# Kernel optimization log

Measured on AMD Instinct MI355X. Metric: run time of the kernel, lower is better.

## Reference

```python
import jax, jax.numpy as jnp
import numpy as np

B, T, E = 2, 2048, 1024
H = 16
DH = E // H  # 64
DFF = 4 * E
EPS = 1e-5


def _layernorm(x, gamma, beta):
    mu = jnp.mean(x, axis=-1, keepdims=True)
    var = jnp.mean((x - mu) ** 2, axis=-1, keepdims=True)
    return (x - mu) * jax.lax.rsqrt(var + EPS) * gamma + beta


def setup_inputs() -> dict:
    key = jax.random.key(0)
    ks = jax.random.split(key, 16)
    s_e = 1.0 / np.sqrt(E)
    s_f = 1.0 / np.sqrt(DFF)
    return {
        "x": jax.random.normal(ks[0], (B, T, E), jnp.float32),
        # per-head QKV projections, stacked over heads [H, E, DH]
        "Wq": jax.random.normal(ks[1], (H, E, DH), jnp.float32) * s_e,
        "bq": jnp.zeros((H, DH), jnp.float32),
        "Wk": jax.random.normal(ks[2], (H, E, DH), jnp.float32) * s_e,
        "bk": jnp.zeros((H, DH), jnp.float32),
        "Wv": jax.random.normal(ks[3], (H, E, DH), jnp.float32) * s_e,
        "bv": jnp.zeros((H, DH), jnp.float32),
        # output projection
        "Wo": jax.random.normal(ks[4], (E, E), jnp.float32) * s_e,
        "bo": jnp.zeros((E,), jnp.float32),
        # feed-forward
        "W1": jax.random.normal(ks[5], (E, DFF), jnp.float32) * s_e,
        "b1": jnp.zeros((DFF,), jnp.float32),
        "W2": jax.random.normal(ks[6], (DFF, E), jnp.float32) * s_f,
        "b2": jnp.zeros((E,), jnp.float32),
        # layernorms
        "gamma1": jnp.ones((E,), jnp.float32),
        "beta1": jnp.zeros((E,), jnp.float32),
        "gamma2": jnp.ones((E,), jnp.float32),
        "beta2": jnp.zeros((E,), jnp.float32),
    }


def reference(x, Wq, bq, Wk, bk, Wv, bv, Wo, bo, W1, b1, W2, b2,
              gamma1, beta1, gamma2, beta2):
    Bc, Tc, Ec = x.shape
    # --- multi-head causal self-attention (dropout = eval/identity) ---
    xn = _layernorm(x, gamma1, beta1)
    q = jnp.einsum('bte,hed->bhtd', xn, Wq) + bq[:, None, :]
    k = jnp.einsum('bte,hed->bhtd', xn, Wk) + bk[:, None, :]
    v = jnp.einsum('bte,hed->bhtd', xn, Wv) + bv[:, None, :]
    scale = 1.0 / np.sqrt(q.shape[-1])
    scores = jnp.einsum('bhtd,bhsd->bhts', q, k) * scale  # [B,H,T,T]
    causal = jnp.tril(jnp.ones((Tc, Tc), bool))
    scores = jnp.where(causal, scores, jnp.float32(-1e9))
    attn = jax.nn.softmax(scores, axis=-1)
    out = jnp.einsum('bhts,bhsd->bhtd', attn, v)          # [B,H,T,DH]
    out = out.transpose(0, 2, 1, 3).reshape(Bc, Tc, Ec)    # concat heads
    out = out @ Wo + bo
    x = x + out
    # --- feed-forward ---
    xn2 = _layernorm(x, gamma2, beta2)
    h = jax.nn.relu(xn2 @ W1 + b1)
    x = x + (h @ W2 + b2)
    return x
```

## Files before the change

kernel.cpp:

```cpp
#include <hip/hip_runtime.h>
#include <stdint.h>

#define BT    4096
#define EDIM  1024
#define TLEN  2048
#define NH    16
#define DHH   64
#define DFFN  4096

typedef short short8 __attribute__((ext_vector_type(8)));
typedef float f32x4  __attribute__((ext_vector_type(4)));

__device__ __forceinline__ float bf2f(unsigned short u) {
    union { unsigned int i; float f; } c; c.i = ((unsigned int)u) << 16; return c.f;
}
__device__ __forceinline__ unsigned short f2bf(float f) {
    union { float f; unsigned int i; } c; c.f = f;
    unsigned int u = c.i;
    unsigned int r = u + 0x7fffu + ((u >> 16) & 1u);
    return (unsigned short)(r >> 16);
}

template<int QKV>
__global__ __launch_bounds__(256) void transpose_kernel(
    const float* src, unsigned short* dst, int Kdim, int srcStride)
{
    __shared__ float T[64][65];
    int t = threadIdx.x;
    int n0 = blockIdx.x * 64, k0 = blockIdx.y * 64;
    int r = t >> 4, c4 = (t & 15) * 4;
    #pragma unroll
    for (int i = 0; i < 4; i++) {
        int rr = r + i * 16;
        const float* p;
        if (QKV) p = src + ((size_t)(n0 >> 6)) * 65536 + (size_t)(k0 + rr) * 64 + c4;
        else     p = src + (size_t)(k0 + rr) * srcStride + n0 + c4;
        float4 v = *(const float4*)p;
        T[c4 + 0][rr] = v.x;
        T[c4 + 1][rr] = v.y;
        T[c4 + 2][rr] = v.z;
        T[c4 + 3][rr] = v.w;
    }
    __syncthreads();
    int rn = t >> 2, ck = (t & 3) * 16;
    short8 o0, o1;
    #pragma unroll
    for (int j = 0; j < 8; j++) o0[j] = (short)f2bf(T[rn][ck + j]);
    #pragma unroll
    for (int j = 0; j < 8; j++) o1[j] = (short)f2bf(T[rn][ck + 8 + j]);
    unsigned short* dp = dst + (size_t)(n0 + rn) * Kdim + k0 + ck;
    *(short8*)dp       = o0;
    *(short8*)(dp + 8) = o1;
}

template<int F32IN>
__global__ __launch_bounds__(256) void ln_stats_kernel(
    const void* __restrict__ x, float* __restrict__ mu_out, float* __restrict__ rstd_out)
{
    int row = blockIdx.x, tid = threadIdx.x;
    size_t off = (size_t)row * EDIM + tid * 4;
    float v0, v1, v2, v3;
    if (F32IN) {
        float4 a = *(const float4*)((const float*)x + off);
        v0 = a.x; v1 = a.y; v2 = a.z; v3 = a.w;
    } else {
        ushort4 raw = *(const ushort4*)((const unsigned short*)x + off);
        v0 = bf2f(raw.x); v1 = bf2f(raw.y); v2 = bf2f(raw.z); v3 = bf2f(raw.w);
    }
    float s  = v0 + v1 + v2 + v3;
    float ss = v0*v0 + v1*v1 + v2*v2 + v3*v3;
    #pragma unroll
    for (int o = 1; o < 64; o <<= 1) {
        s  += __shfl_xor(s,  o, 64);
        ss += __shfl_xor(ss, o, 64);
    }
    __shared__ float red[8];
    int wave = tid >> 6;
    if ((tid & 63) == 0) { red[wave*2] = s; red[wave*2+1] = ss; }
    __syncthreads();
    if (tid == 0) {
        s  = red[0] + red[2] + red[4] + red[6];
        ss = red[1] + red[3] + red[5] + red[7];
        float mu  = s * (1.0f / EDIM);
        float var = ss * (1.0f / EDIM) - mu * mu;
        mu_out[row]   = mu;
        rstd_out[row] = rsqrtf(var + 1e-5f);
    }
}

template<int F32IN>
__global__ __launch_bounds__(256) void ln_apply_kernel(
    const void* __restrict__ x, const float* __restrict__ mu, const float* __restrict__ rstd,
    const float* __restrict__ g, const float* __restrict__ b, unsigned short* __restrict__ out)
{
    int row = blockIdx.x, tid = threadIdx.x;
    float m = mu[row], rs = rstd[row];
    size_t off = (size_t)row * EDIM + tid * 4;
    float v0, v1, v2, v3;
    if (F32IN) {
        float4 a = *(const float4*)((const float*)x + off);
        v0 = a.x; v1 = a.y; v2 = a.z; v3 = a.w;
    } else {
        ushort4 raw = *(const ushort4*)((const unsigned short*)x + off);
        v0 = bf2f(raw.x); v1 = bf2f(raw.y); v2 = bf2f(raw.z); v3 = bf2f(raw.w);
    }
    float4 gv = *(const float4*)(g + tid * 4);
    float4 bv = *(const float4*)(b + tid * 4);
    ushort4 o;
    o.x = f2bf((v0 - m) * rs * gv.x + bv.x);
    o.y = f2bf((v1 - m) * rs * gv.y + bv.y);
    o.z = f2bf((v2 - m) * rs * gv.z + bv.z);
    o.w = f2bf((v3 - m) * rs * gv.w + bv.w);
    *(ushort4*)(out + off) = o;
}

#define V_QKV  0
#define V_WO   1
#define V_FF1  2
#define V_FF2A 3
#define V_FF2B 4
#define LDKK 72

template<int VARIANT, int BN>
__global__ __launch_bounds__(256) void gemm_bt_kernel(
    const unsigned short* A,
    const unsigned short* Bt,
    const float* bias,
    const void* resid,
    void* out,
    int N, int K)
{
    constexpr int NJ = BN / 32;
    __shared__ __align__(16) unsigned short As[128 * LDKK];
    __shared__ __align__(16) unsigned short Bs[BN * LDKK];
    int tid  = threadIdx.x;
    int lane = tid & 63, wave = tid >> 6;
    int quad = lane >> 4, l16 = lane & 15;
    int wr = wave >> 1, wc = wave & 1;
    int m0 = blockIdx.y * 128, n0 = blockIdx.x * BN;

    f32x4 acc[4][NJ];
    #pragma unroll
    for (int i = 0; i < 4; i++)
        #pragma unroll
        for (int j = 0; j < NJ; j++) acc[i][j] = (f32x4){0.f, 0.f, 0.f, 0.f};

    int rowA = tid >> 1, colA = (tid & 1) * 32;
    int rowB, colB;
    if (BN == 128) { rowB = tid >> 1; colB = (tid & 1) * 32; }
    else           { rowB = tid >> 2; colB = (tid & 3) * 16; }

    for (int k0 = 0; k0 < K; k0 += 64) {
        const unsigned short* ap = A + (size_t)(m0 + rowA) * K + k0 + colA;
        short8 a0 = *(const short8*)ap;
        short8 a1 = *(const short8*)(ap + 8);
        short8 a2 = *(const short8*)(ap + 16);
        short8 a3 = *(const short8*)(ap + 24);
        const unsigned short* bp = Bt + (size_t)(n0 + rowB) * K + k0 + colB;
        short8 b0 = *(const short8*)bp;
        short8 b1 = *(const short8*)(bp + 8);
        short8 b2, b3;
        if (BN == 128) {
            b2 = *(const short8*)(bp + 16);
            b3 = *(const short8*)(bp + 24);
        }

        *(short8*)(&As[rowA * LDKK + colA])      = a0;
        *(short8*)(&As[rowA * LDKK + colA + 8])  = a1;
        *(short8*)(&As[rowA * LDKK + colA + 16]) = a2;
        *(short8*)(&As[rowA * LDKK + colA + 24]) = a3;
        *(short8*)(&Bs[rowB * LDKK + colB])      = b0;
        *(short8*)(&Bs[rowB * LDKK + colB + 8])  = b1;
        if (BN == 128) {
            *(short8*)(&Bs[rowB * LDKK + colB + 16]) = b2;
            *(short8*)(&Bs[rowB * LDKK + colB + 24]) = b3;
        }

        __syncthreads();

        #pragma unroll
        for (int ks = 0; ks < 2; ks++) {
            short8 af[4], bf[NJ];
            #pragma unroll
            for (int i = 0; i < 4; i++)
                af[i] = *(const short8*)(&As[(wr * 64 + i * 16 + l16) * LDKK + ks * 32 + quad * 8]);
            #pragma unroll
            for (int j = 0; j < NJ; j++)
                bf[j] = *(const short8*)(&Bs[(wc * (BN / 2) + j * 16 + l16) * LDKK + ks * 32 + quad * 8]);
            #pragma unroll
            for (int i = 0; i < 4; i++)
                #pragma unroll
                for (int j = 0; j < NJ; j++)
                    acc[i][j] = __builtin_amdgcn_mfma_f32_16x16x32_bf16(af[i], bf[j], acc[i][j], 0, 0, 0);
        }

        __syncthreads();
    }

    #pragma unroll
    for (int j = 0; j < NJ; j++) {
        int c = n0 + wc * (BN / 2) + j * 16 + l16;
        float bi = (VARIANT == V_FF2A) ? 0.0f : bias[c];
        #pragma unroll
        for (int i = 0; i < 4; i++) {
            #pragma unroll
            for (int r = 0; r < 4; r++) {
                int m = m0 + wr * 64 + i * 16 + quad * 4 + r;
                float val = acc[i][j][r] + bi;
                if (VARIANT == V_WO)
                    val += ((const float*)resid)[(size_t)m * N + c];
                if (VARIANT == V_FF2B)
                    val += bf2f(((const unsigned short*)resid)[(size_t)m * N + c])
                         + ((const float*)out)[(size_t)m * N + c];
                if (VARIANT == V_FF1)
                    val = fmaxf(val, 0.0f);
                if (VARIANT == V_QKV) {
                    int b = m >> 11, t = m & 2047, h = c >> 6, d = c & 63;
                    ((unsigned short*)out)[(((size_t)(b * NH + h)) * TLEN + t) * DHH + d] = f2bf(val);
                } else if (VARIANT == V_FF2A || VARIANT == V_FF2B) {
                    ((float*)out)[(size_t)m * N + c] = val;
                } else {
                    ((unsigned short*)out)[(size_t)m * N + c] = f2bf(val);
                }
            }
        }
    }
}

__global__ __launch_bounds__(256) void attn_kernel(
    const unsigned short* __restrict__ q,
    const unsigned short* __restrict__ k,
    const unsigned short* __restrict__ v,
    unsigned short* __restrict__ att)
{
    __shared__ __align__(16) unsigned short Ks[64 * 72];
    __shared__ __align__(16) unsigned short Vt[64 * 72];
    __shared__ __align__(16) unsigned short Ps[4][16 * 72];
    int tid  = threadIdx.x;
    int lane = tid & 63, wave = tid >> 6;
    int quad = lane >> 4, l16 = lane & 15;
    int bh = blockIdx.x;
    int q0 = blockIdx.y * 64;
    int qw = q0 + wave * 16;

    const unsigned short* Qb = q + ((size_t)bh * TLEN + qw) * DHH;
    const unsigned short* Kb = k + (size_t)bh * TLEN * DHH;
    const unsigned short* Vb = v + (size_t)bh * TLEN * DHH;

    short8 aq0 = *(const short8*)(Qb + l16 * DHH + quad * 8);
    short8 aq1 = *(const short8*)(Qb + l16 * DHH + 32 + quad * 8);

    f32x4 o[4];
    #pragma unroll
    for (int n = 0; n < 4; n++) o[n] = (f32x4){0.f, 0.f, 0.f, 0.f};
    f32x4 mrow = {-1e30f, -1e30f, -1e30f, -1e30f};
    f32x4 lrow = {0.f, 0.f, 0.f, 0.f};
    unsigned short* Pw = Ps[wave];

    int krow = tid >> 2, kcol = (tid & 3) * 16;
    int vsl  = tid >> 5, vd2  = (tid & 31) * 2;

    int nch = blockIdx.y + 1;
    for (int ch = 0; ch < nch; ch++) {
        int s0 = ch * 64;
        __syncthreads();
        {
            const unsigned short* kp = Kb + (size_t)(s0 + krow) * DHH + kcol;
            *(short8*)(&Ks[krow * 72 + kcol])     = *(const short8*)kp;
            *(short8*)(&Ks[krow * 72 + kcol + 8]) = *(const short8*)(kp + 8);
        }
        #pragma unroll
        for (int i = 0; i < 8; i++) {
            int sl = vsl + i * 8;
            ushort2 w = *(const ushort2*)(Vb + (size_t)(s0 + sl) * DHH + vd2);
            Vt[vd2 * 72 + sl]       = w.x;
            Vt[(vd2 + 1) * 72 + sl] = w.y;
        }
        __syncthreads();

        f32x4 S[4];
        #pragma unroll
        for (int n = 0; n < 4; n++) {
            S[n] = (f32x4){0.f, 0.f, 0.f, 0.f};
            short8 b0 = *(const short8*)(&Ks[(n * 16 + l16) * 72 + quad * 8]);
            short8 b1 = *(const short8*)(&Ks[(n * 16 + l16) * 72 + 32 + quad * 8]);
            S[n] = __builtin_amdgcn_mfma_f32_16x16x32_bf16(aq0, b0, S[n], 0, 0, 0);
            S[n] = __builtin_amdgcn_mfma_f32_16x16x32_bf16(aq1, b1, S[n], 0, 0, 0);
        }

        int qbase = qw + quad * 4;
        #pragma unroll
        for (int r = 0; r < 4; r++) {
            float xv[4];
            #pragma unroll
            for (int n = 0; n < 4; n++) {
                float xx = S[n][r] * 0.125f;
                if (s0 + n * 16 + l16 > qbase + r) xx = -1e30f;
                xv[n] = xx;
            }
            float mx = fmaxf(fmaxf(xv[0], xv[1]), fmaxf(xv[2], xv[3]));
            mx = fmaxf(mx, __shfl_xor(mx, 1, 64));
            mx = fmaxf(mx, __shfl_xor(mx, 2, 64));
            mx = fmaxf(mx, __shfl_xor(mx, 4, 64));
            mx = fmaxf(mx, __shfl_xor(mx, 8, 64));
            float mnew  = fmaxf(mrow[r], mx);
            float alpha = __expf(mrow[r] - mnew);
            float p0 = __expf(xv[0] - mnew);
            float p1 = __expf(xv[1] - mnew);
            float p2 = __expf(xv[2] - mnew);
            float p3 = __expf(xv[3] - mnew);
            float rs = (p0 + p1) + (p2 + p3);
            rs += __shfl_xor(rs, 1, 64);
            rs += __shfl_xor(rs, 2, 64);
            rs += __shfl_xor(rs, 4, 64);
            rs += __shfl_xor(rs, 8, 64);
            lrow[r] = lrow[r] * alpha + rs;
            mrow[r] = mnew;
            #pragma unroll
            for (int n = 0; n < 4; n++) o[n][r] *= alpha;
            int prow = (quad * 4 + r) * 72;
            Pw[prow + l16]      = f2bf(p0);
            Pw[prow + 16 + l16] = f2bf(p1);
            Pw[prow + 32 + l16] = f2bf(p2);
            Pw[prow + 48 + l16] = f2bf(p3);
        }
        __syncthreads();

        short8 ap0 = *(const short8*)(Pw + l16 * 72 + quad * 8);
        short8 ap1 = *(const short8*)(Pw + l16 * 72 + 32 + quad * 8);
        #pragma unroll
        for (int n = 0; n < 4; n++) {
            short8 b0 = *(const short8*)(&Vt[(n * 16 + l16) * 72 + quad * 8]);
            short8 b1 = *(const short8*)(&Vt[(n * 16 + l16) * 72 + 32 + quad * 8]);
            o[n] = __builtin_amdgcn_mfma_f32_16x16x32_bf16(ap0, b0, o[n], 0, 0, 0);
            o[n] = __builtin_amdgcn_mfma_f32_16x16x32_bf16(ap1, b1, o[n], 0, 0, 0);
        }
    }

    int bidx = bh >> 4, hh = bh & 15;
    #pragma unroll
    for (int r = 0; r < 4; r++) {
        int t = qw + quad * 4 + r;
        size_t rowoff = ((size_t)(bidx * TLEN + t)) * EDIM + hh * 64;
        float inv = 1.0f / lrow[r];
        #pragma unroll
        for (int n = 0; n < 4; n++)
            att[rowoff + n * 16 + l16] = f2bf(o[n][r] * inv);
    }
}

extern "C" void kernel_launch(void* const* d_in, const int* in_sizes, int n_in,
                              void* d_out, int out_size, void* d_ws, size_t ws_size,
                              hipStream_t stream)
{
    (void)in_sizes; (void)n_in; (void)out_size; (void)ws_size;
    const float* x   = (const float*)d_in[0];
    const float* Wq  = (const float*)d_in[1];
    const float* bq  = (const float*)d_in[2];
    const float* Wk  = (const float*)d_in[3];
    const float* bk  = (const float*)d_in[4];
    const float* Wv  = (const float*)d_in[5];
    const float* bv  = (const float*)d_in[6];
    const float* Wo  = (const float*)d_in[7];
    const float* bo  = (const float*)d_in[8];
    const float* W1  = (const float*)d_in[9];
    const float* b1  = (const float*)d_in[10];
    const float* W2  = (const float*)d_in[11];
    const float* b2  = (const float*)d_in[12];
    const float* g1  = (const float*)d_in[13];
    const float* be1 = (const float*)d_in[14];
    const float* g2  = (const float*)d_in[15];
    const float* be2 = (const float*)d_in[16];

    unsigned short* ws  = (unsigned short*)d_ws;
    unsigned short* xn  = ws;
    unsigned short* qb  = ws + 4194304;
    unsigned short* kb  = ws + 8388608;
    unsigned short* vb  = ws + 12582912;
    unsigned short* wqt = ws + 16777216;
    unsigned short* wkt = ws + 17825792;
    unsigned short* wvt = ws + 18874368;
    unsigned short* att = ws + 16777216;
    unsigned short* x1  = ws + 4194304;
    unsigned short* wot = ws + 8388608;
    unsigned short* w1t = ws + 8388608;
    unsigned short* w2t = ws + 10485760;
    unsigned short* hb  = ws + 12582912;
    float* mu1 = (float*)((char*)d_ws + 41943040);
    float* rs1 = mu1 + 4096;
    float* mu2 = mu1 + 8192;
    float* rs2 = mu1 + 12288;

    dim3 gT64(16, 16);
    dim3 gE(EDIM / 64, BT / 128);
    dim3 gF(2048 / 128, BT / 128);

    transpose_kernel<1><<<gT64, 256, 0, stream>>>(Wq, wqt, EDIM, 64);
    transpose_kernel<1><<<gT64, 256, 0, stream>>>(Wk, wkt, EDIM, 64);
    transpose_kernel<1><<<gT64, 256, 0, stream>>>(Wv, wvt, EDIM, 64);

    ln_stats_kernel<1><<<BT, 256, 0, stream>>>(x, mu1, rs1);
    ln_apply_kernel<1><<<BT, 256, 0, stream>>>(x, mu1, rs1, g1, be1, xn);

    gemm_bt_kernel<V_QKV, 64><<<gE, 256, 0, stream>>>(xn, wqt, bq, nullptr, qb, EDIM, EDIM);
    gemm_bt_kernel<V_QKV, 64><<<gE, 256, 0, stream>>>(xn, wkt, bk, nullptr, kb, EDIM, EDIM);
    gemm_bt_kernel<V_QKV, 64><<<gE, 256, 0, stream>>>(xn, wvt, bv, nullptr, vb, EDIM, EDIM);

    attn_kernel<<<dim3(NH * 2, TLEN / 64), 256, 0, stream>>>(qb, kb, vb, att);

    transpose_kernel<0><<<gT64, 256, 0, stream>>>(Wo, wot, EDIM, EDIM);
    gemm_bt_kernel<V_WO, 64><<<gE, 256, 0, stream>>>(att, wot, bo, x, x1, EDIM, EDIM);

    ln_stats_kernel<0><<<BT, 256, 0, stream>>>(x1, mu2, rs2);
    ln_apply_kernel<0><<<BT, 256, 0, stream>>>(x1, mu2, rs2, g2, be2, xn);

    transpose_kernel<0><<<dim3(32, 16), 256, 0, stream>>>(W1, w1t, EDIM, DFFN);
    transpose_kernel<0><<<dim3(16, 32), 256, 0, stream>>>(W2, w2t, 2048, EDIM);
    gemm_bt_kernel<V_FF1, 128><<<gF, 256, 0, stream>>>(xn, w1t, b1, nullptr, hb, 2048, EDIM);
    gemm_bt_kernel<V_FF2A, 64><<<gE, 256, 0, stream>>>(hb, w2t, nullptr, nullptr, d_out, EDIM, 2048);
    transpose_kernel<0><<<dim3(32, 16), 256, 0, stream>>>(W1 + 2048, w1t, EDIM, DFFN);
    transpose_kernel<0><<<dim3(16, 32), 256, 0, stream>>>(W2 + (size_t)2048 * EDIM, w2t, 2048, EDIM);
    gemm_bt_kernel<V_FF1, 128><<<gF, 256, 0, stream>>>(xn, w1t, b1 + 2048, nullptr, hb, 2048, EDIM);
    gemm_bt_kernel<V_FF2B, 64><<<gE, 256, 0, stream>>>(hb, w2t, b2, x1, d_out, EDIM, 2048);
}
```

Baseline: 495.5 us.

## Restructure attention: pre-transposed V, direct global operand loads, lazy rescale, XCD-aware scheduling

Adds a separate kernel that transposes V into a [bh, d, t] layout so the attention kernel can load MFMA B operands for K and V straight from global memory. This removes the shared-memory staging of K/V and the block-wide barriers. The attention loop now processes 128-key chunks per wave. It skips masking on fully visible chunks and uses exp2 with a prescaled log2e constant. It rescales the running output only when the row max grows by more than a threshold, and sums the row sum across lanes once at the end. Blocks are remapped so heads group per XCD and the longest causal tiles launch first. The cost is an extra kernel launch and V round-trip through memory, plus more global/L2 traffic for K/V loads that each wave repeats without reuse through LDS.

```diff
diff --git a/kernel.cpp b/kernel.cpp
--- a/kernel.cpp
+++ b/kernel.cpp
@@ -19,6 +19,13 @@
     unsigned int u = c.i;
     unsigned int r = u + 0x7fffu + ((u >> 16) & 1u);
     return (unsigned short)(r >> 16);
+}
+__device__ __forceinline__ float fexp2(float x) {
+#if __has_builtin(__builtin_amdgcn_exp2f)
+    return __builtin_amdgcn_exp2f(x);
+#else
+    return __expf(x * 0.69314718056f);
+#endif
 }
 
 template<int QKV>
@@ -51,6 +58,30 @@
     unsigned short* dp = dst + (size_t)(n0 + rn) * Kdim + k0 + ck;
     *(short8*)dp       = o0;
     *(short8*)(dp + 8) = o1;
+}
+
+__global__ __launch_bounds__(256) void vtrans_kernel(
+    const unsigned short* __restrict__ v, unsigned short* __restrict__ vt)
+{
+    __shared__ __align__(16) unsigned short T[64][72];
+    int bh = blockIdx.x, st = blockIdx.y;
+    int t = threadIdx.x;
+    int r = t >> 2, c = (t & 3) * 16;
+    const unsigned short* src = v + ((size_t)bh * TLEN + st * 64) * DHH;
+    short8 a0 = *(const short8*)(src + r * DHH + c);
+    short8 a1 = *(const short8*)(src + r * DHH + c + 8);
+    *(short8*)&T[r][c]     = a0;
+    *(short8*)&T[r][c + 8] = a1;
+    __syncthreads();
+    int d = t >> 2;
+    short8 o0, o1;
+    #pragma unroll
+    for (int j = 0; j < 8; j++) o0[j] = (short)T[c + j][d];
+    #pragma unroll
+    for (int j = 0; j < 8; j++) o1[j] = (short)T[c + 8 + j][d];
+    unsigned short* dst = vt + ((size_t)bh * DHH + d) * TLEN + st * 64 + c;
+    *(short8*)dst       = o0;
+    *(short8*)(dst + 8) = o1;
 }
 
 template<int F32IN>
@@ -230,22 +261,23 @@
 __global__ __launch_bounds__(256) void attn_kernel(
     const unsigned short* __restrict__ q,
     const unsigned short* __restrict__ k,
-    const unsigned short* __restrict__ v,
+    const unsigned short* __restrict__ vt,
     unsigned short* __restrict__ att)
 {
-    __shared__ __align__(16) unsigned short Ks[64 * 72];
-    __shared__ __align__(16) unsigned short Vt[64 * 72];
-    __shared__ __align__(16) unsigned short Ps[4][16 * 72];
+    __shared__ __align__(16) unsigned short Ps[4][16 * 136];
     int tid  = threadIdx.x;
     int lane = tid & 63, wave = tid >> 6;
     int quad = lane >> 4, l16 = lane & 15;
-    int bh = blockIdx.x;
-    int q0 = blockIdx.y * 64;
-    int qw = q0 + wave * 16;
-
-    const unsigned short* Qb = q + ((size_t)bh * TLEN + qw) * DHH;
-    const unsigned short* Kb = k + (size_t)bh * TLEN * DHH;
-    const unsigned short* Vb = v + (size_t)bh * TLEN * DHH;
+
+    int flat = blockIdx.x;
+    int xcd  = flat & 7, idx = flat >> 3;
+    int bh   = xcd * 4 + (idx >> 5);
+    int qt   = 31 - (idx & 31);
+    int qw   = qt * 64 + wave * 16;
+
+    const unsigned short* Qb = q  + ((size_t)bh * TLEN + qw) * DHH;
+    const unsigned short* Kb = k  + (size_t)bh * TLEN * DHH;
+    const unsigned short* Vb = vt + (size_t)bh * DHH * TLEN;
 
     short8 aq0 = *(const short8*)(Qb + l16 * DHH + quad * 8);
     short8 aq1 = *(const short8*)(Qb + l16 * DHH + 32 + quad * 8);
@@ -256,93 +288,86 @@
     f32x4 mrow = {-1e30f, -1e30f, -1e30f, -1e30f};
     f32x4 lrow = {0.f, 0.f, 0.f, 0.f};
     unsigned short* Pw = Ps[wave];
-
-    int krow = tid >> 2, kcol = (tid & 3) * 16;
-    int vsl  = tid >> 5, vd2  = (tid & 31) * 2;
-
-    int nch = blockIdx.y + 1;
+    const float cs = 0.18033688011f;
+
+    int nch = (qw + 16 + 127) >> 7;
     for (int ch = 0; ch < nch; ch++) {
-        int s0 = ch * 64;
-        __syncthreads();
-        {
-            const unsigned short* kp = Kb + (size_t)(s0 + krow) * DHH + kcol;
-            *(short8*)(&Ks[krow * 72 + kcol])     = *(const short8*)kp;
-            *(short8*)(&Ks[krow * 72 + kcol + 8]) = *(const short8*)(kp + 8);
-        }
-        #pragma unroll
-        for (int i = 0; i < 8; i++) {
-            int sl = vsl + i * 8;
-            ushort2 w = *(const ushort2*)(Vb + (size_t)(s0 + sl) * DHH + vd2);
-            Vt[vd2 * 72 + sl]       = w.x;
-            Vt[(vd2 + 1) * 72 + sl] = w.y;
-        }
-        __syncthreads();
-
-        f32x4 S[4];
-        #pragma unroll
-        for (int n = 0; n < 4; n++) {
-            S[n] = (f32x4){0.f, 0.f, 0.f, 0.f};
-            short8 b0 = *(const short8*)(&Ks[(n * 16 + l16) * 72 + quad * 8]);
-            short8 b1 = *(const short8*)(&Ks[(n * 16 + l16) * 72 + 32 + quad * 8]);
-            S[n] = __builtin_amdgcn_mfma_f32_16x16x32_bf16(aq0, b0, S[n], 0, 0, 0);
-            S[n] = __builtin_amdgcn_mfma_f32_16x16x32_bf16(aq1, b1, S[n], 0, 0, 0);
-        }
-
-        int qbase = qw + quad * 4;
+        int s0 = ch * 128;
+        f32x4 S[8];
+        #pragma unroll
+        for (int n = 0; n < 8; n++) {
+            const unsigned short* kp = Kb + (size_t)(s0 + n * 16 + l16) * DHH + quad * 8;
+            short8 b0 = *(const short8*)kp;
+            short8 b1 = *(const short8*)(kp + 32);
+            f32x4 s = (f32x4){0.f, 0.f, 0.f, 0.f};
+            s = __builtin_amdgcn_mfma_f32_16x16x32_bf16(aq0, b0, s, 0, 0, 0);
+            s = __builtin_amdgcn_mfma_f32_16x16x32_bf16(aq1, b1, s, 0, 0, 0);
+            S[n] = s;
+        }
+        bool needmask = (s0 + 127 > qw);
         #pragma unroll
         for (int r = 0; r < 4; r++) {
-            float xv[4];
-            #pragma unroll
-            for (int n = 0; n < 4; n++) {
-                float xx = S[n][r] * 0.125f;
-                if (s0 + n * 16 + l16 > qbase + r) xx = -1e30f;
+            float xv[8];
+            #pragma unroll
+            for (int n = 0; n < 8; n++) {
+                float xx = S[n][r] * cs;
+                if (needmask && (s0 + n * 16 + l16 > qw + quad * 4 + r)) xx = -1e30f;
                 xv[n] = xx;
             }
-            float mx = fmaxf(fmaxf(xv[0], xv[1]), fmaxf(xv[2], xv[3]));
+            float mx = fmaxf(fmaxf(fmaxf(xv[0], xv[1]), fmaxf(xv[2], xv[3])),
+                             fmaxf(fmaxf(xv[4], xv[5]), fmaxf(xv[6], xv[7])));
             mx = fmaxf(mx, __shfl_xor(mx, 1, 64));
             mx = fmaxf(mx, __shfl_xor(mx, 2, 64));
             mx = fmaxf(mx, __shfl_xor(mx, 4, 64));
             mx = fmaxf(mx, __shfl_xor(mx, 8, 64));
-            float mnew  = fmaxf(mrow[r], mx);
-            float alpha = __expf(mrow[r] - mnew);
-            float p0 = __expf(xv[0] - mnew);
-            float p1 = __expf(xv[1] - mnew);
-            float p2 = __expf(xv[2] - mnew);
-            float p3 = __expf(xv[3] - mnew);
-            float rs = (p0 + p1) + (p2 + p3);
-            rs += __shfl_xor(rs, 1, 64);
-            rs += __shfl_xor(rs, 2, 64);
-            rs += __shfl_xor(rs, 4, 64);
-            rs += __shfl_xor(rs, 8, 64);
-            lrow[r] = lrow[r] * alpha + rs;
-            mrow[r] = mnew;
-            #pragma unroll
-            for (int n = 0; n < 4; n++) o[n][r] *= alpha;
-            int prow = (quad * 4 + r) * 72;
-            Pw[prow + l16]      = f2bf(p0);
-            Pw[prow + 16 + l16] = f2bf(p1);
-            Pw[prow + 32 + l16] = f2bf(p2);
-            Pw[prow + 48 + l16] = f2bf(p3);
-        }
-        __syncthreads();
-
-        short8 ap0 = *(const short8*)(Pw + l16 * 72 + quad * 8);
-        short8 ap1 = *(const short8*)(Pw + l16 * 72 + 32 + quad * 8);
+            float used;
+            if (__all(mx <= mrow[r] + 8.0f)) {
+                used = mrow[r];
+            } else {
+                float mnew  = fmaxf(mrow[r], mx);
+                float alpha = fexp2(mrow[r] - mnew);
+                lrow[r] *= alpha;
+                o[0][r] *= alpha; o[1][r] *= alpha;
+                o[2][r] *= alpha; o[3][r] *= alpha;
+                mrow[r] = mnew;
+                used = mnew;
+            }
+            float ps = 0.f;
+            int prow = (quad * 4 + r) * 136;
+            #pragma unroll
+            for (int n = 0; n < 8; n++) {
+                float p = fexp2(xv[n] - used);
+                ps += p;
+                Pw[prow + n * 16 + l16] = f2bf(p);
+            }
+            lrow[r] += ps;
+        }
+        short8 ap[4];
+        #pragma unroll
+        for (int ks = 0; ks < 4; ks++)
+            ap[ks] = *(const short8*)(Pw + l16 * 136 + ks * 32 + quad * 8);
         #pragma unroll
         for (int n = 0; n < 4; n++) {
-            short8 b0 = *(const short8*)(&Vt[(n * 16 + l16) * 72 + quad * 8]);
-            short8 b1 = *(const short8*)(&Vt[(n * 16 + l16) * 72 + 32 + quad * 8]);
-            o[n] = __builtin_amdgcn_mfma_f32_16x16x32_bf16(ap0, b0, o[n], 0, 0, 0);
-            o[n] = __builtin_amdgcn_mfma_f32_16x16x32_bf16(ap1, b1, o[n], 0, 0, 0);
+            const unsigned short* vp = Vb + (size_t)(n * 16 + l16) * TLEN + s0 + quad * 8;
+            #pragma unroll
+            for (int ks = 0; ks < 4; ks++) {
+                short8 b = *(const short8*)(vp + ks * 32);
+                o[n] = __builtin_amdgcn_mfma_f32_16x16x32_bf16(ap[ks], b, o[n], 0, 0, 0);
+            }
         }
     }
 
     int bidx = bh >> 4, hh = bh & 15;
     #pragma unroll
     for (int r = 0; r < 4; r++) {
+        float ls = lrow[r];
+        ls += __shfl_xor(ls, 1, 64);
+        ls += __shfl_xor(ls, 2, 64);
+        ls += __shfl_xor(ls, 4, 64);
+        ls += __shfl_xor(ls, 8, 64);
+        float inv = 1.0f / ls;
         int t = qw + quad * 4 + r;
         size_t rowoff = ((size_t)(bidx * TLEN + t)) * EDIM + hh * 64;
-        float inv = 1.0f / lrow[r];
         #pragma unroll
         for (int n = 0; n < 4; n++)
             att[rowoff + n * 16 + l16] = f2bf(o[n][r] * inv);
@@ -374,6 +399,7 @@
 
     unsigned short* ws  = (unsigned short*)d_ws;
     unsigned short* xn  = ws;
+    unsigned short* vtg = ws;
     unsigned short* qb  = ws + 4194304;
     unsigned short* kb  = ws + 8388608;
     unsigned short* vb  = ws + 12582912;
@@ -406,7 +432,9 @@
     gemm_bt_kernel<V_QKV, 64><<<gE, 256, 0, stream>>>(xn, wkt, bk, nullptr, kb, EDIM, EDIM);
     gemm_bt_kernel<V_QKV, 64><<<gE, 256, 0, stream>>>(xn, wvt, bv, nullptr, vb, EDIM, EDIM);
 
-    attn_kernel<<<dim3(NH * 2, TLEN / 64), 256, 0, stream>>>(qb, kb, vb, att);
+    vtrans_kernel<<<dim3(NH * 2, TLEN / 64), 256, 0, stream>>>(vb, vtg);
+
+    attn_kernel<<<dim3(1024), 256, 0, stream>>>(qb, kb, vtg, att);
 
     transpose_kernel<0><<<gT64, 256, 0, stream>>>(Wo, wot, EDIM, EDIM);
     gemm_bt_kernel<V_WO, 64><<<gE, 256, 0, stream>>>(att, wot, bo, x, x1, EDIM, EDIM);
```

Measured after the change: 552.0 us. +11.4%, slower.
